# Performance work log

Hardware: AMD Instinct MI355X
Metric: run time of the kernel (lower is better)

Reference implementation:

```python
import jax, jax.numpy as jnp
import numpy as np

GN_GROUPS = 32
GN_EPS = 1e-5


def _conv3x3(x, w, b):
    # NCHW 3x3 conv, stride 1, pad 1
    y = jax.lax.conv_general_dilated(x, w, (1, 1), [(1, 1), (1, 1)],
                                     dimension_numbers=('NCHW', 'OIHW', 'NCHW'))
    return y + b[None, :, None, None]


def _bilinear(x, py, px):
    # x: [N,C,H,W]; py,px: [N,H,W] fractional sample coords; zeros outside.
    N, C, H, W = x.shape
    y0 = jnp.floor(py)
    x0 = jnp.floor(px)
    wy = py - y0
    wx = px - x0
    xf = x.reshape(N, C, H * W)
    out = jnp.zeros((N, C, H, W), x.dtype)
    corners = ((y0, x0, (1 - wy) * (1 - wx)),
               (y0, x0 + 1, (1 - wy) * wx),
               (y0 + 1, x0, wy * (1 - wx)),
               (y0 + 1, x0 + 1, wy * wx))
    for yy, xx, w in corners:
        valid = ((yy >= 0) & (yy <= H - 1) & (xx >= 0) & (xx <= W - 1)).astype(x.dtype)
        yi = jnp.clip(yy, 0, H - 1).astype(jnp.int32)
        xi = jnp.clip(xx, 0, W - 1).astype(jnp.int32)
        idx = (yi * W + xi).reshape(N, 1, H * W)
        g = jnp.take_along_axis(xf, idx, axis=2).reshape(N, C, H, W)
        out = out + g * (w * valid)[:, None]
    return out


def setup_inputs() -> dict:
    key = jax.random.key(0)
    ks = jax.random.split(key, 8)
    N, C, H, W = 4, 128, 160, 160
    s = 0.05
    return {
        'x': jax.random.normal(ks[0], (N, C, H, W), jnp.float32),
        'w_tm': jax.random.normal(ks[1], (4, C, 3, 3), jnp.float32) * s,
        'b_tm': jax.random.normal(ks[2], (4,), jnp.float32) * s,
        'w_tr': jax.random.normal(ks[3], (2, C, 3, 3), jnp.float32) * s,
        'b_tr': jax.random.normal(ks[4], (2,), jnp.float32) * s,
        'w_dcn': jax.random.normal(ks[5], (C, C, 3, 3), jnp.float32) * s,
        'gn_gamma': jnp.ones((C,), jnp.float32),
        'gn_beta': jnp.zeros((C,), jnp.float32),
    }


def reference(x, w_tm, b_tm, w_tr, b_tr, w_dcn, gn_gamma, gn_beta):
    N, C, H, W = x.shape
    Cout = w_dcn.shape[0]
    # regular 3x3 grid offsets: row0 = ky, row1 = kx, k ordered ky-major
    R = jnp.array([[-1., -1., -1., 0., 0., 0., 1., 1., 1.],
                   [-1., 0., 1., -1., 0., 1., -1., 0., 1.]], x.dtype)
    tm = _conv3x3(x, w_tm, b_tm)   # [N,4,H,W] -> per-pixel 2x2 affine
    tr = _conv3x3(x, w_tr, b_tr)   # [N,2,H,W] -> per-pixel (dy,dx) translation
    tmm = tm.transpose(0, 2, 3, 1).reshape(N, H, W, 2, 2)
    off = jnp.einsum('nhwij,jk->nhwik', tmm, R) - R  # [N,H,W,2,9]
    dy = off[:, :, :, 0, :] + tr[:, 0][..., None]    # [N,H,W,9]
    dx = off[:, :, :, 1, :] + tr[:, 1][..., None]
    hh = jnp.arange(H, dtype=x.dtype)[None, :, None, None]
    ww = jnp.arange(W, dtype=x.dtype)[None, None, :, None]
    kk = jnp.arange(9)
    ky = (kk // 3).astype(x.dtype)
    kx = (kk % 3).astype(x.dtype)
    py = hh - 1.0 + ky + dy  # stride=1, pad=1, dilation=1
    px = ww - 1.0 + kx + dx
    wk = w_dcn.reshape(Cout, C, 9)
    out = jnp.zeros((N, Cout, H, W), x.dtype)
    for k in range(9):  # fixed small loop over kernel points
        s = _bilinear(x, py[..., k], px[..., k])
        out = out + jnp.einsum('nchw,oc->nohw', s, wk[:, :, k])
    # GroupNorm
    og = out.reshape(N, GN_GROUPS, (Cout // GN_GROUPS) * H * W)
    mu = og.mean(axis=2, keepdims=True)
    var = og.var(axis=2, keepdims=True)
    og = (og - mu) * jax.lax.rsqrt(var + GN_EPS)
    out = og.reshape(N, Cout, H, W) * gn_gamma[None, :, None, None] + gn_beta[None, :, None, None]
    return jax.nn.relu(out + x)
```

## Files before the change

### kernel.cpp

```cpp
#include <hip/hip_runtime.h>
#include <hip/hip_fp16.h>
#include <math.h>

#define Hh 160
#define Ww 160
#define Cc 128
#define HW 25600
#define NPIX 102400

typedef __attribute__((ext_vector_type(8))) _Float16 half8;
typedef __attribute__((ext_vector_type(4))) float f32x4;
typedef __attribute__((ext_vector_type(4))) unsigned int u32x4;

union h2u { __half2 h; unsigned int u; };

#define WS_OFFS 0u
#define WS_WA   7372800u
#define WS_GSUM 7667712u
#define WS_GSQ  7668224u
#define WS_XT   7668736u
#define WS_RAW  33883136u

__global__ void wtrans_kernel(const float* __restrict__ w_dcn,
                              unsigned short* __restrict__ wA) {
    int idx = blockIdx.x * 256 + threadIdx.x;
    if (idx >= 9 * 128 * 128) return;
    int k = idx >> 14;
    int o = (idx >> 7) & 127;
    int c = idx & 127;
    wA[idx] = __half_as_ushort(__float2half(w_dcn[(o * 128 + c) * 9 + k]));
}

__global__ void __launch_bounds__(256) xpose_kernel(
    const float* __restrict__ x, unsigned short* __restrict__ xT) {
    __shared__ float L[128 * 65];
    int b = blockIdx.x;
    int n = b / 400;
    int px0 = (b - n * 400) * 64;
    int t = threadIdx.x;
    const float* xn = x + (size_t)n * Cc * HW + px0;
#pragma unroll
    for (int i = 0; i < 32; ++i) {
        int idx = i * 256 + t;
        int ch = idx >> 6;
        int pxl = idx & 63;
        L[ch * 65 + pxl] = xn[(size_t)ch * HW + pxl];
    }
    __syncthreads();
    unsigned short* dst = xT + ((size_t)n * HW + px0) * 128;
#pragma unroll
    for (int j = 0; j < 16; ++j) {
        int idx = j * 256 + t;
        int pxl = idx >> 6;
        int cp = idx & 63;
        h2u cv;
        cv.h = __floats2half2_rn(L[(2 * cp) * 65 + pxl],
                                 L[(2 * cp + 1) * 65 + pxl]);
        *(unsigned int*)(dst + (size_t)pxl * 128 + cp * 2) = cv.u;
    }
}

__global__ void __launch_bounds__(256) offs_kernel(
    const float* __restrict__ x, const float* __restrict__ w_tm,
    const float* __restrict__ b_tm, const float* __restrict__ w_tr,
    const float* __restrict__ b_tr, float* __restrict__ offs2) {
    __shared__ float wt[128 * 9 * 8];
    int t = threadIdx.x;
    for (int idx = t; idx < 6912; idx += 256) {
        int j = idx % 6;
        int rest = idx / 6;
        int tap = rest % 9;
        int c = rest / 9;
        float v = (j < 4) ? w_tm[(j * 128 + c) * 9 + tap]
                          : w_tr[((j - 4) * 128 + c) * 9 + tap];
        wt[rest * 8 + j] = v;
    }
    __syncthreads();
    int bid = blockIdx.x;
    int blk = (bid & 7) * 50 + (bid >> 3);
    int p = blk * 256 + t;
    int n = p / HW;
    int hw = p - n * HW;
    int h = hw / Ww;
    int w = hw - h * Ww;
    int addr[9];
    float msk[9];
#pragma unroll
    for (int tap = 0; tap < 9; ++tap) {
        int dy = tap / 3 - 1, dx = tap % 3 - 1;
        int yy = h + dy, xx = w + dx;
        bool v = (yy >= 0) && (yy < Hh) && (xx >= 0) && (xx < Ww);
        addr[tap] = v ? yy * Ww + xx : 0;
        msk[tap] = v ? 1.f : 0.f;
    }
    float a0 = 0, a1 = 0, a2 = 0, a3 = 0, a4 = 0, a5 = 0;
    const float* xn = x + n * Cc * HW;
#pragma unroll 2
    for (int c = 0; c < Cc; ++c) {
        const float* xc = xn + c * HW;
#pragma unroll
        for (int tap = 0; tap < 9; ++tap) {
            float v = msk[tap] * xc[addr[tap]];
            const float* wp = &wt[(c * 9 + tap) * 8];
            float4 w4 = *(const float4*)wp;
            float2 w2 = *(const float2*)(wp + 4);
            a0 += v * w4.x; a1 += v * w4.y; a2 += v * w4.z; a3 += v * w4.w;
            a4 += v * w2.x; a5 += v * w2.y;
        }
    }
    a0 += b_tm[0]; a1 += b_tm[1]; a2 += b_tm[2]; a3 += b_tm[3];
    a4 += b_tr[0]; a5 += b_tr[1];
#pragma unroll
    for (int k = 0; k < 9; ++k) {
        float r0 = (float)(k / 3) - 1.f;
        float r1 = (float)(k % 3) - 1.f;
        float2 st;
        st.x = (float)h + a0 * r0 + a1 * r1 + a4;
        st.y = (float)w + a2 * r0 + a3 * r1 + a5;
        *(float2*)(offs2 + ((size_t)k * NPIX + p) * 2) = st;
    }
}

__global__ void __launch_bounds__(256, 4) dcn2_kernel(
    const unsigned short* __restrict__ xT, const float* __restrict__ offs2,
    const unsigned short* __restrict__ wA, float* __restrict__ raw,
    float* __restrict__ gsum, float* __restrict__ gsq) {
    __shared__ __align__(16) unsigned short Bt[64 * 128];
    int t = threadIdx.x;
    int lane = t & 63;
    int wid = t >> 6;
    int wm = wid & 1, wn = wid >> 1;
    int quad = lane >> 4, l15 = lane & 15;
    int sub = lane >> 4;
    int s = lane & 15;

    int bid = blockIdx.x;
    int blk = (bid & 7) * 200 + (bid >> 3);
    int px0 = blk * 64;
    int n = px0 / HW;
    int hw0 = px0 - n * HW;
    const unsigned short* xb = xT + (size_t)n * HW * 128;
    const char* Ag = (const char*)wA;
    const float2* offv = (const float2*)offs2;
    int pbase = px0 + wid * 16 + sub;
    int sb = s << 3;

    f32x4 acc[4][2];
#pragma unroll
    for (int i = 0; i < 4; ++i)
#pragma unroll
        for (int j = 0; j < 2; ++j) acc[i][j] = (f32x4)0.f;

    float2 pc[4], pcn[4];
    u32x4 v00[2], v01[2], v10[2], v11[2];
    float w00[2], w01[2], w10[2], w11[2];

#define ISSUE(sl, r) do {                                                   \
    float py_ = pc[r].x, px_ = pc[r].y;                                     \
    float y0f_ = floorf(py_), x0f_ = floorf(px_);                           \
    float fy_ = py_ - y0f_, fx_ = px_ - x0f_;                               \
    int y0_ = (int)y0f_, xi0_ = (int)x0f_;                                  \
    int y1_ = y0_ + 1, xi1_ = xi0_ + 1;                                     \
    float wa_ = (1.f - fy_) * (1.f - fx_), wb_ = (1.f - fy_) * fx_;         \
    float wc_ = fy_ * (1.f - fx_), wd_ = fy_ * fx_;                         \
    bool vy0_ = (unsigned)y0_ < (unsigned)Hh;                               \
    bool vy1_ = (unsigned)y1_ < (unsigned)Hh;                               \
    bool vx0_ = (unsigned)xi0_ < (unsigned)Ww;                              \
    bool vx1_ = (unsigned)xi1_ < (unsigned)Ww;                              \
    w00[sl] = (vy0_ && vx0_) ? wa_ : 0.f;                                   \
    w01[sl] = (vy0_ && vx1_) ? wb_ : 0.f;                                   \
    w10[sl] = (vy1_ && vx0_) ? wc_ : 0.f;                                   \
    w11[sl] = (vy1_ && vx1_) ? wd_ : 0.f;                                   \
    int cy0_ = vy0_ ? y0_ : 0, cy1_ = vy1_ ? y1_ : 0;                       \
    int cx0_ = vx0_ ? xi0_ : 0, cx1_ = vx1_ ? xi1_ : 0;                     \
    v00[sl] = *(const u32x4*)(xb + ((size_t)(cy0_ * Ww + cx0_) << 7) + sb); \
    v01[sl] = *(const u32x4*)(xb + ((size_t)(cy0_ * Ww + cx1_) << 7) + sb); \
    v10[sl] = *(const u32x4*)(xb + ((size_t)(cy1_ * Ww + cx0_) << 7) + sb); \
    v11[sl] = *(const u32x4*)(xb + ((size_t)(cy1_ * Ww + cx1_) << 7) + sb); \
} while (0)

#define COMBINE(sl, r) do {                                                 \
    int p_ = wid * 16 + (r) * 4 + sub;                                      \
    __half2 W00_ = __float2half2_rn(w00[sl]);                               \
    __half2 W01_ = __float2half2_rn(w01[sl]);                               \
    __half2 W10_ = __float2half2_rn(w10[sl]);                               \
    __half2 W11_ = __float2half2_rn(w11[sl]);                               \
    u32x4 outv_;                                                            \
    _Pragma("unroll")                                                       \
    for (int e = 0; e < 4; ++e) {                                           \
        h2u a_, b_, c_, d_, o_;                                             \
        a_.u = v00[sl][e]; b_.u = v01[sl][e];                               \
        c_.u = v10[sl][e]; d_.u = v11[sl][e];                               \
        __half2 t_ = __hmul2(W11_, d_.h);                                   \
        t_ = __hfma2(W10_, c_.h, t_);                                       \
        t_ = __hfma2(W01_, b_.h, t_);                                       \
        t_ = __hfma2(W00_, a_.h, t_);                                       \
        o_.h = t_;                                                          \
        outv_[e] = o_.u;                                                    \
    }                                                                       \
    *(u32x4*)&Bt[p_ * 128 + ((s ^ (p_ & 15)) << 3)] = outv_;                \
} while (0)

#pragma unroll
    for (int r = 0; r < 4; ++r) pc[r] = offv[pbase + r * 4];

    for (int k = 0; k < 9; ++k) {
        __syncthreads();

        if (k < 8) {
#pragma unroll
            for (int r = 0; r < 4; ++r)
                pcn[r] = offv[(size_t)(k + 1) * NPIX + pbase + r * 4];
        }

        ISSUE(0, 0); ISSUE(1, 1);
        COMBINE(0, 0); COMBINE(1, 1);
        ISSUE(0, 2); ISSUE(1, 3);
        COMBINE(0, 2); COMBINE(1, 3);
        __syncthreads();

#pragma unroll
        for (int q = 0; q < 4; ++q) {
            half8 a[4], b[2];
#pragma unroll
            for (int i = 0; i < 4; ++i)
                a[i] = *(const half8*)(Ag +
                        ((size_t)(k * 128 + wm * 64 + i * 16 + l15) << 8) +
                        q * 64 + quad * 16);
#pragma unroll
            for (int j = 0; j < 2; ++j) {
                int row = wn * 32 + j * 16 + l15;
                int ur = (q * 4 + quad) ^ (row & 15);
                b[j] = *(const half8*)&Bt[row * 128 + ur * 8];
            }
#pragma unroll
            for (int i = 0; i < 4; ++i)
#pragma unroll
                for (int j = 0; j < 2; ++j)
                    acc[i][j] = __builtin_amdgcn_mfma_f32_16x16x32_f16(
                        a[i], b[j], acc[i][j], 0, 0, 0);
        }

        if (k < 8) {
#pragma unroll
            for (int r = 0; r < 4; ++r) pc[r] = pcn[r];
        }
    }

#undef ISSUE
#undef COMBINE

    size_t rbase = ((size_t)n * Cc) * HW + hw0;
#pragma unroll
    for (int i = 0; i < 4; ++i) {
        float s_i = 0.f, q_i = 0.f;
#pragma unroll
        for (int j = 0; j < 2; ++j) {
            int pxl = wn * 32 + j * 16 + l15;
#pragma unroll
            for (int rr = 0; rr < 4; ++rr) {
                int o = wm * 64 + i * 16 + quad * 4 + rr;
                float v = acc[i][j][rr];
                raw[rbase + (size_t)o * HW + pxl] = v;
                s_i += v;
                q_i += v * v;
            }
        }
#pragma unroll
        for (int m = 1; m < 16; m <<= 1) {
            s_i += __shfl_xor(s_i, m);
            q_i += __shfl_xor(q_i, m);
        }
        if (l15 == 0) {
            int g = wm * 16 + i * 4 + quad;
            atomicAdd(&gsum[n * 32 + g], s_i);
            atomicAdd(&gsq[n * 32 + g], q_i);
        }
    }
}

__global__ void __launch_bounds__(256) finish_kernel(
    const float* __restrict__ raw, const float* __restrict__ x,
    const float* __restrict__ gsum, const float* __restrict__ gsq,
    const float* __restrict__ gamma, const float* __restrict__ beta,
    float* __restrict__ out) {
    int i = blockIdx.x * 256 + threadIdx.x;
    int e = i * 4;
    int n = e / (Cc * HW);
    int rem = e - n * (Cc * HW);
    int c = rem / HW;
    int g = c >> 2;
    const float inv = 1.f / 102400.f;
    float mu = gsum[n * 32 + g] * inv;
    float var = gsq[n * 32 + g] * inv - mu * mu;
    float rs = rsqrtf(var + 1e-5f);
    float sc = gamma[c] * rs;
    float sh = beta[c] - mu * sc;
    float4 v = *(const float4*)&raw[e];
    float4 xv = *(const float4*)&x[e];
    float4 r;
    r.x = fmaxf(v.x * sc + sh + xv.x, 0.f);
    r.y = fmaxf(v.y * sc + sh + xv.y, 0.f);
    r.z = fmaxf(v.z * sc + sh + xv.z, 0.f);
    r.w = fmaxf(v.w * sc + sh + xv.w, 0.f);
    *(float4*)&out[e] = r;
}

extern "C" void kernel_launch(void* const* d_in, const int* in_sizes, int n_in,
                              void* d_out, int out_size, void* d_ws, size_t ws_size,
                              hipStream_t stream) {
    const float* x      = (const float*)d_in[0];
    const float* w_tm   = (const float*)d_in[1];
    const float* b_tm   = (const float*)d_in[2];
    const float* w_tr   = (const float*)d_in[3];
    const float* b_tr   = (const float*)d_in[4];
    const float* w_dcn  = (const float*)d_in[5];
    const float* gamma  = (const float*)d_in[6];
    const float* beta   = (const float*)d_in[7];
    char* ws = (char*)d_ws;
    float*          offs2 = (float*)(ws + WS_OFFS);
    unsigned short* wA    = (unsigned short*)(ws + WS_WA);
    float*          gsum  = (float*)(ws + WS_GSUM);
    float*          gsq   = (float*)(ws + WS_GSQ);
    unsigned short* xT    = (unsigned short*)(ws + WS_XT);
    float*          raw   = (float*)(ws + WS_RAW);
    float* out = (float*)d_out;

    (void)hipMemsetAsync(gsum, 0, 1024, stream);
    wtrans_kernel<<<576, 256, 0, stream>>>(w_dcn, wA);
    xpose_kernel<<<1600, 256, 0, stream>>>(x, xT);
    offs_kernel<<<400, 256, 0, stream>>>(x, w_tm, b_tm, w_tr, b_tr, offs2);
    dcn2_kernel<<<1600, 256, 0, stream>>>(xT, offs2, wA, raw, gsum, gsq);
    finish_kernel<<<12800, 256, 0, stream>>>(raw, x, gsum, gsq, gamma, beta, out);
}
```

Before: 389.4 us.

## Give each wave private double-buffered pixel tile and overlap gather with MFMA

```diff
diff --git a/kernel.cpp b/kernel.cpp
--- a/kernel.cpp
+++ b/kernel.cpp
@@ -121,37 +121,37 @@
     }
 }
 
-__global__ void __launch_bounds__(256, 4) dcn2_kernel(
+__global__ void __launch_bounds__(256, 2) dcn2_kernel(
     const unsigned short* __restrict__ xT, const float* __restrict__ offs2,
     const unsigned short* __restrict__ wA, float* __restrict__ raw,
     float* __restrict__ gsum, float* __restrict__ gsq) {
-    __shared__ __align__(16) unsigned short Bt[64 * 128];
+    __shared__ __align__(16) unsigned short Bt[4 * 2 * 32 * 128];
     int t = threadIdx.x;
     int lane = t & 63;
     int wid = t >> 6;
-    int wm = wid & 1, wn = wid >> 1;
     int quad = lane >> 4, l15 = lane & 15;
     int sub = lane >> 4;
     int s = lane & 15;
 
     int bid = blockIdx.x;
-    int blk = (bid & 7) * 200 + (bid >> 3);
-    int px0 = blk * 64;
+    int blk = (bid & 7) * 100 + (bid >> 3);
+    int px0 = blk * 128;
     int n = px0 / HW;
     int hw0 = px0 - n * HW;
     const unsigned short* xb = xT + (size_t)n * HW * 128;
     const char* Ag = (const char*)wA;
     const float2* offv = (const float2*)offs2;
-    int pbase = px0 + wid * 16 + sub;
+    int pbase = px0 + wid * 32 + sub;
     int sb = s << 3;
-
-    f32x4 acc[4][2];
-#pragma unroll
-    for (int i = 0; i < 4; ++i)
+    int wbase = wid * (2 * 32 * 128);
+
+    f32x4 acc[8][2];
+#pragma unroll
+    for (int i = 0; i < 8; ++i)
 #pragma unroll
         for (int j = 0; j < 2; ++j) acc[i][j] = (f32x4)0.f;
 
-    float2 pc[4], pcn[4];
+    float2 pc[8], pcn[8];
     u32x4 v00[2], v01[2], v10[2], v11[2];
     float w00[2], w01[2], w10[2], w11[2];
 
@@ -179,8 +179,8 @@
     v11[sl] = *(const u32x4*)(xb + ((size_t)(cy1_ * Ww + cx1_) << 7) + sb); \
 } while (0)
 
-#define COMBINE(sl, r) do {                                                 \
-    int p_ = wid * 16 + (r) * 4 + sub;                                      \
+#define COMBINE(sl, r, bB) do {                                             \
+    int p_ = (r) * 4 + sub;                                                 \
     __half2 W00_ = __float2half2_rn(w00[sl]);                               \
     __half2 W01_ = __float2half2_rn(w01[sl]);                               \
     __half2 W10_ = __float2half2_rn(w10[sl]);                               \
@@ -198,68 +198,75 @@
         o_.h = t_;                                                          \
         outv_[e] = o_.u;                                                    \
     }                                                                       \
-    *(u32x4*)&Bt[p_ * 128 + ((s ^ (p_ & 15)) << 3)] = outv_;                \
+    *(u32x4*)&Bt[(bB) + p_ * 128 + ((s ^ (p_ & 15)) << 3)] = outv_;         \
 } while (0)
 
-#pragma unroll
-    for (int r = 0; r < 4; ++r) pc[r] = offv[pbase + r * 4];
+#define QPHASE(q, ra, rb) do {                                              \
+    half8 a_[8];                                                            \
+    _Pragma("unroll")                                                       \
+    for (int i = 0; i < 8; ++i)                                             \
+        a_[i] = *(const half8*)(Ag +                                        \
+                ((size_t)(k * 128 + i * 16 + l15) << 8) +                   \
+                (q) * 64 + quad * 16);                                      \
+    if (k < 8) { ISSUE(0, ra); ISSUE(1, rb); }                              \
+    half8 b0_, b1_;                                                         \
+    {                                                                       \
+        int ur_ = ((q) * 4 + quad) ^ l15;                                   \
+        b0_ = *(const half8*)&Bt[rB + l15 * 128 + ur_ * 8];                 \
+        b1_ = *(const half8*)&Bt[rB + (16 + l15) * 128 + ur_ * 8];          \
+    }                                                                       \
+    _Pragma("unroll")                                                       \
+    for (int i = 0; i < 8; ++i) {                                           \
+        acc[i][0] = __builtin_amdgcn_mfma_f32_16x16x32_f16(                 \
+            a_[i], b0_, acc[i][0], 0, 0, 0);                                \
+        acc[i][1] = __builtin_amdgcn_mfma_f32_16x16x32_f16(                 \
+            a_[i], b1_, acc[i][1], 0, 0, 0);                                \
+    }                                                                       \
+    if (k < 8) { COMBINE(0, ra, wB); COMBINE(1, rb, wB); }                  \
+} while (0)
+
+#pragma unroll
+    for (int r = 0; r < 8; ++r) pc[r] = offv[pbase + r * 4];
+    ISSUE(0, 0); ISSUE(1, 1); COMBINE(0, 0, wbase); COMBINE(1, 1, wbase);
+    ISSUE(0, 2); ISSUE(1, 3); COMBINE(0, 2, wbase); COMBINE(1, 3, wbase);
+    ISSUE(0, 4); ISSUE(1, 5); COMBINE(0, 4, wbase); COMBINE(1, 5, wbase);
+    ISSUE(0, 6); ISSUE(1, 7); COMBINE(0, 6, wbase); COMBINE(1, 7, wbase);
+#pragma unroll
+    for (int r = 0; r < 8; ++r)
+        pc[r] = offv[(size_t)1 * NPIX + pbase + r * 4];
 
     for (int k = 0; k < 9; ++k) {
-        __syncthreads();
-
-        if (k < 8) {
-#pragma unroll
-            for (int r = 0; r < 4; ++r)
-                pcn[r] = offv[(size_t)(k + 1) * NPIX + pbase + r * 4];
-        }
-
-        ISSUE(0, 0); ISSUE(1, 1);
-        COMBINE(0, 0); COMBINE(1, 1);
-        ISSUE(0, 2); ISSUE(1, 3);
-        COMBINE(0, 2); COMBINE(1, 3);
-        __syncthreads();
-
-#pragma unroll
-        for (int q = 0; q < 4; ++q) {
-            half8 a[4], b[2];
-#pragma unroll
-            for (int i = 0; i < 4; ++i)
-                a[i] = *(const half8*)(Ag +
-                        ((size_t)(k * 128 + wm * 64 + i * 16 + l15) << 8) +
-                        q * 64 + quad * 16);
-#pragma unroll
-            for (int j = 0; j < 2; ++j) {
-                int row = wn * 32 + j * 16 + l15;
-                int ur = (q * 4 + quad) ^ (row & 15);
-                b[j] = *(const half8*)&Bt[row * 128 + ur * 8];
-            }
-#pragma unroll
-            for (int i = 0; i < 4; ++i)
-#pragma unroll
-                for (int j = 0; j < 2; ++j)
-                    acc[i][j] = __builtin_amdgcn_mfma_f32_16x16x32_f16(
-                        a[i], b[j], acc[i][j], 0, 0, 0);
-        }
-
-        if (k < 8) {
-#pragma unroll
-            for (int r = 0; r < 4; ++r) pc[r] = pcn[r];
+        int rB = wbase + (k & 1) * (32 * 128);
+        int wB = wbase + ((k + 1) & 1) * (32 * 128);
+        QPHASE(0, 0, 1);
+        if (k < 7) {
+#pragma unroll
+            for (int r = 0; r < 8; ++r)
+                pcn[r] = offv[(size_t)(k + 2) * NPIX + pbase + r * 4];
+        }
+        QPHASE(1, 2, 3);
+        QPHASE(2, 4, 5);
+        QPHASE(3, 6, 7);
+        if (k < 7) {
+#pragma unroll
+            for (int r = 0; r < 8; ++r) pc[r] = pcn[r];
         }
     }
 
 #undef ISSUE
 #undef COMBINE
+#undef QPHASE
 
     size_t rbase = ((size_t)n * Cc) * HW + hw0;
 #pragma unroll
-    for (int i = 0; i < 4; ++i) {
+    for (int i = 0; i < 8; ++i) {
         float s_i = 0.f, q_i = 0.f;
 #pragma unroll
         for (int j = 0; j < 2; ++j) {
-            int pxl = wn * 32 + j * 16 + l15;
+            int pxl = wid * 32 + j * 16 + l15;
 #pragma unroll
             for (int rr = 0; rr < 4; ++rr) {
-                int o = wm * 64 + i * 16 + quad * 4 + rr;
+                int o = i * 16 + quad * 4 + rr;
                 float v = acc[i][j][rr];
                 raw[rbase + (size_t)o * HW + pxl] = v;
                 s_i += v;
@@ -272,7 +279,7 @@
             q_i += __shfl_xor(q_i, m);
         }
         if (l15 == 0) {
-            int g = wm * 16 + i * 4 + quad;
+            int g = i * 4 + quad;
             atomicAdd(&gsum[n * 32 + g], s_i);
             atomicAdd(&gsq[n * 32 + g], q_i);
         }
@@ -330,6 +337,6 @@
     wtrans_kernel<<<576, 256, 0, stream>>>(w_dcn, wA);
     xpose_kernel<<<1600, 256, 0, stream>>>(x, xT);
     offs_kernel<<<400, 256, 0, stream>>>(x, w_tm, b_tm, w_tr, b_tr, offs2);
-    dcn2_kernel<<<1600, 256, 0, stream>>>(xT, offs2, wA, raw, gsum, gsq);
+    dcn2_kernel<<<800, 256, 0, stream>>>(xT, offs2, wA, raw, gsum, gsq);
     finish_kernel<<<12800, 256, 0, stream>>>(raw, x, gsum, gsq, gamma, beta, out);
 }
```

Result: slower. 400.5 us (+2.8%).
